# Kernel tuning notes

Measured on AMD Instinct MI355X. Metric: run time of the kernel, lower is better.

## Reference

```python
import jax, jax.numpy as jnp
import numpy as np

N_HEADS = 2

def setup_inputs() -> dict:
    key = jax.random.key(0)
    ks = jax.random.split(key, 10)
    d, bank, b, t = 192, 1000, 16, 4096
    s = 1.0 / np.sqrt(d)
    return {
        "z": jax.random.normal(ks[0], (b, d, t), jnp.float32),
        "memory_bank": jax.random.normal(ks[1], (d, bank), jnp.float32),
        "Wq": jax.random.normal(ks[2], (d, d), jnp.float32) * s,
        "bq": jax.random.normal(ks[3], (d,), jnp.float32) * 0.02,
        "Wk": jax.random.normal(ks[4], (d, d), jnp.float32) * s,
        "bk": jax.random.normal(ks[5], (d,), jnp.float32) * 0.02,
        "Wv": jax.random.normal(ks[6], (d, d), jnp.float32) * s,
        "bv": jax.random.normal(ks[7], (d,), jnp.float32) * 0.02,
        "Wo": jax.random.normal(ks[8], (d, d), jnp.float32) * s,
        "bo": jax.random.normal(ks[9], (d,), jnp.float32) * 0.02,
    }


def _split_heads(x):
    # x: [b, d, t] -> [b, h, t, dk]  (matches view(b, h, dk, t).transpose(2, 3))
    b, d, t = x.shape
    dk = d // N_HEADS
    return x.reshape(b, N_HEADS, dk, t).transpose(0, 1, 3, 2)


def reference(z, memory_bank, Wq, bq, Wk, bk, Wv, bv, Wo, bo):
    b, d, t = z.shape
    dk = d // N_HEADS
    # memory bank expanded over batch: [b, d, bank]
    c = jnp.broadcast_to(memory_bank[None], (b,) + memory_bank.shape)
    # 1x1 conv projections == per-channel linear
    q = jnp.einsum('oc,bct->bot', Wq, z) + bq[None, :, None]
    k = jnp.einsum('oc,bcs->bos', Wk, c) + bk[None, :, None]
    v = jnp.einsum('oc,bcs->bos', Wv, c) + bv[None, :, None]
    qh = _split_heads(q)  # [b, h, t, dk]
    kh = _split_heads(k)  # [b, h, bank, dk]
    vh = _split_heads(v)  # [b, h, bank, dk]
    scores = jnp.einsum('bhtd,bhsd->bhts', qh, kh) / jnp.sqrt(jnp.asarray(dk, z.dtype))
    p = jax.nn.softmax(scores, axis=-1)  # [b, h, t, bank]
    out = jnp.einsum('bhts,bhsd->bhtd', p, vh)  # [b, h, t, dk]
    out = out.transpose(0, 1, 3, 2).reshape(b, d, t)  # merge heads -> [b, d, t]
    return jnp.einsum('oc,bct->bot', Wo, out) + bo[None, :, None]
```

## Files before the change

### kernel.cpp

```cpp
#include <hip/hip_runtime.h>


typedef float  f32x4  __attribute__((ext_vector_type(4)));
typedef __bf16 bf16;
typedef __bf16 bf16x4 __attribute__((ext_vector_type(4)));
typedef __bf16 bf16x8 __attribute__((ext_vector_type(8)));

#define B_   16
#define D_   192
#define T_   4096
#define BANK 1000
#define SP   1024
#define DK   96
#define SCALE 0.10206207261596577f
#define LOG2E 1.4426950408889634f

__global__ __launch_bounds__(256) void pre_kernel(
    const float* __restrict__ z, bf16* __restrict__ zT,
    const float* __restrict__ mb,
    const float* __restrict__ Wk, const float* __restrict__ bk,
    const float* __restrict__ Wv, const float* __restrict__ bv,
    bf16* __restrict__ ktg, bf16* __restrict__ vtg) {
  __shared__ __align__(16) bf16 sT[64 * 200];
  const int tid = threadIdx.x;
  if (blockIdx.y < 16) {
    const int t0 = blockIdx.x * 64, b = blockIdx.y;
#pragma unroll
    for (int it = 0; it < 48; ++it) {
      int e = tid + 256 * it;
      int c = e >> 6, tl = e & 63;
      sT[tl * 200 + c] = (bf16)z[((size_t)b * D_ + c) * T_ + t0 + tl];
    }
    __syncthreads();
#pragma unroll
    for (int it = 0; it < 6; ++it) {
      int g = tid + 256 * it;
      int tl = g / 24, c8 = (g % 24) * 8;
      bf16x8 v = *(const bf16x8*)&sT[tl * 200 + c8];
      *(bf16x8*)&zT[((size_t)b * T_ + t0 + tl) * D_ + c8] = v;
    }
  } else {
    int idx = (blockIdx.y - 16) * 64 + blockIdx.x;
    int s = (idx & 3) * 256 + tid;
    int o = idx >> 2;
    int h = o / DK, i = o % DK;
    float ak = 0.f, av = 0.f;
    if (s < BANK) {
      ak = bk[o]; av = bv[o];
      for (int c = 0; c < D_; ++c) {
        float m = mb[c * BANK + s];
        ak += Wk[o * D_ + c] * m;
        av += Wv[o * D_ + c] * m;
      }
    }
    ktg[(size_t)(h * SP + s) * DK + i] = (bf16)ak;
    vtg[(size_t)(h * DK + i) * SP + s] = (bf16)av;
  }
}

template <typename OT>
__global__ __launch_bounds__(256) void proj_kernel(
    const bf16* __restrict__ XT, const float* __restrict__ W,
    const float* __restrict__ bias, OT* __restrict__ Y, float outscale) {
  __shared__ __align__(16) char smem[24576];
  bf16* sB = (bf16*)smem;
  float* sE = (float*)smem;

  const int tid = threadIdx.x;
  const int t0 = blockIdx.x * 256, o0 = blockIdx.y * 64, b = blockIdx.z;
  const int lane = tid & 63, wv = tid >> 6;
  const int quad = lane >> 4, l15 = lane & 15;

  const bf16* ap[4];
#pragma unroll
  for (int m = 0; m < 4; ++m)
    ap[m] = &XT[((size_t)b * T_ + t0 + (wv * 4 + m) * 16 + l15) * D_ + quad * 8];
  bf16x8 acur[4];
#pragma unroll
  for (int m = 0; m < 4; ++m) acur[m] = *(const bf16x8*)ap[m];

#pragma unroll
  for (int r = 0; r < 6; ++r) {
    int g = tid + 256 * r;
    int kb = g >> 8, nt = (g >> 6) & 3, qd = (g >> 4) & 3, l5 = g & 15;
    const float* wp = &W[(o0 + nt * 16 + l5) * D_ + kb * 32 + qd * 8];
    f32x4 wa = *(const f32x4*)wp, wb = *(const f32x4*)(wp + 4);
    bf16x8 pk;
#pragma unroll
    for (int u = 0; u < 4; ++u) { pk[u] = (bf16)wa[u]; pk[4 + u] = (bf16)wb[u]; }
    *(bf16x8*)&sB[(size_t)g * 8] = pk;
  }

  f32x4 acc[4][4];
#pragma unroll
  for (int m = 0; m < 4; ++m)
#pragma unroll
    for (int n = 0; n < 4; ++n) acc[m][n] = (f32x4){0.f, 0.f, 0.f, 0.f};

  __syncthreads();
  for (int kb = 0; kb < 6; ++kb) {
    bf16x8 anext[4];
    if (kb < 5) {
#pragma unroll
      for (int m = 0; m < 4; ++m)
        anext[m] = *(const bf16x8*)(ap[m] + (kb + 1) * 32);
    }
    bf16x8 bf[4];
#pragma unroll
    for (int n = 0; n < 4; ++n)
      bf[n] = *(const bf16x8*)&sB[(size_t)((kb * 4 + n) * 64 + lane) * 8];
#pragma unroll
    for (int m = 0; m < 4; ++m)
#pragma unroll
      for (int n = 0; n < 4; ++n)
        acc[m][n] = __builtin_amdgcn_mfma_f32_16x16x32_bf16(acur[m], bf[n], acc[m][n], 0, 0, 0);
    if (kb < 5) {
#pragma unroll
      for (int m = 0; m < 4; ++m) acur[m] = anext[m];
    }
  }
  __syncthreads();

  float bs[4];
#pragma unroll
  for (int n = 0; n < 4; ++n) bs[n] = bias[o0 + n * 16 + l15];
  float* se = sE + wv * 1088;
#pragma unroll
  for (int m = 0; m < 4; ++m) {
#pragma unroll
    for (int n = 0; n < 4; ++n)
#pragma unroll
      for (int r = 0; r < 4; ++r)
        se[(quad * 4 + r) * 68 + n * 16 + l15] = (acc[m][n][r] + bs[n]) * outscale;
#pragma unroll
    for (int oo = 0; oo < 16; ++oo) {
      int ol = oo * 4 + quad;
      Y[((size_t)b * D_ + o0 + ol) * T_ + t0 + wv * 64 + m * 16 + l15] =
          (OT)se[l15 * 68 + ol];
    }
  }
}

__global__ __launch_bounds__(512) void attn_kernel(
    const bf16* __restrict__ zT, const float* __restrict__ Wq,
    const float* __restrict__ bq, const bf16* __restrict__ ktg,
    const bf16* __restrict__ vtg, bf16* __restrict__ owsT) {
  __shared__ __align__(16) char smem[32768];
  bf16* kt = (bf16*)smem;
  bf16* vt = (bf16*)(smem + 12288);
  bf16* sP = (bf16*)(smem + 24576);
  bf16* qt = (bf16*)smem;

  const int tid = threadIdx.x;
  const int t0 = blockIdx.x * 128, h = blockIdx.y, b = blockIdx.z;
  const int lane = tid & 63, wv = tid >> 6;
  const int quad = lane >> 4, l15 = lane & 15;

  const bf16* kb_g = ktg + (size_t)h * SP * DK;
  const bf16* vb_g = vtg + (size_t)h * DK * SP;
  const bf16* sp_ptr[3];
  int sp_str[3];
#pragma unroll
  for (int r = 0; r < 3; ++r) {
    int g = tid + 512 * r;
    if (g < 768) {
      int kb = g >> 8, n = (g >> 6) & 3, qd = (g >> 4) & 3, l5 = g & 15;
      sp_ptr[r] = kb_g + (size_t)(n * 16 + l5) * DK + kb * 32 + qd * 8;
      sp_str[r] = 64 * DK;
    } else {
      int gv = g - 768, blk = gv >> 6;
      int kbv = blk / 6, n = blk % 6, qd = (gv >> 4) & 3, l5 = gv & 15;
      sp_ptr[r] = vb_g + (size_t)(n * 16 + l5) * SP + kbv * 32 + qd * 8;
      sp_str[r] = 64;
    }
  }
  bf16x8 kreg[3];
#pragma unroll
  for (int r = 0; r < 3; ++r) kreg[r] = *(const bf16x8*)sp_ptr[r];

  f32x4 qacc[6];
#pragma unroll
  for (int n = 0; n < 6; ++n) qacc[n] = (f32x4){0.f, 0.f, 0.f, 0.f};
  const bf16*  zrow = &zT[((size_t)b * T_ + t0 + wv * 16 + l15) * D_ + quad * 8];
  const float* wrow = &Wq[(size_t)(h * DK + l15) * D_ + quad * 8];
  for (int kb = 0; kb < 6; ++kb) {
    bf16x8 zf = *(const bf16x8*)(zrow + kb * 32);
#pragma unroll
    for (int n = 0; n < 6; ++n) {
      const float* wp = wrow + (size_t)n * 16 * D_ + kb * 32;
      f32x4 wa = *(const f32x4*)wp, wb = *(const f32x4*)(wp + 4);
      bf16x8 wf;
#pragma unroll
      for (int u = 0; u < 4; ++u) { wf[u] = (bf16)wa[u]; wf[4 + u] = (bf16)wb[u]; }
      qacc[n] = __builtin_amdgcn_mfma_f32_16x16x32_bf16(wf, zf, qacc[n], 0, 0, 0);
    }
  }
#pragma unroll
  for (int n = 0; n < 6; ++n) {
    f32x4 bq4 = *(const f32x4*)&bq[h * DK + n * 16 + quad * 4];
    int g = ((n & 1) * 2 + (quad >> 1)) * 16 + l15;
    int gs = g ^ ((g >> 3) & 7);
    bf16x4 pk;
#pragma unroll
    for (int r = 0; r < 4; ++r)
      pk[r] = (bf16)((qacc[n][r] + bq4[r]) * (SCALE * LOG2E));
    *(bf16x4*)&qt[(size_t)(((n >> 1) * 8 + wv) * 64 + gs) * 8 + (quad & 1) * 4] = pk;
  }
  bf16x8 qf[3];
#pragma unroll
  for (int kb = 0; kb < 3; ++kb)
    qf[kb] = *(const bf16x8*)&qt[(size_t)((kb * 8 + wv) * 64 + (lane ^ ((lane >> 3) & 7))) * 8];

  f32x4 oaccT[6];
#pragma unroll
  for (int n = 0; n < 6; ++n) oaccT[n] = (f32x4){0.f, 0.f, 0.f, 0.f};
  float m_run = -1e30f, l_run = 0.f;

  for (int ch = 0; ch < 16; ++ch) {
    __syncthreads();
#pragma unroll
    for (int r = 0; r < 3; ++r)
      *(bf16x8*)(smem + (size_t)(tid + 512 * r) * 16) = kreg[r];
    __syncthreads();
    if (ch < 15) {
#pragma unroll
      for (int r = 0; r < 3; ++r) {
        sp_ptr[r] += sp_str[r];
        kreg[r] = *(const bf16x8*)sp_ptr[r];
      }
    }

    f32x4 scT[4];
#pragma unroll
    for (int n = 0; n < 4; ++n) scT[n] = (f32x4){0.f, 0.f, 0.f, 0.f};
#pragma unroll
    for (int kb = 0; kb < 3; ++kb) {
#pragma unroll
      for (int n = 0; n < 4; ++n) {
        bf16x8 kf = *(const bf16x8*)&kt[(size_t)((kb * 4 + n) * 64 + lane) * 8];
        scT[n] = __builtin_amdgcn_mfma_f32_16x16x32_bf16(kf, qf[kb], scT[n], 0, 0, 0);
      }
    }
    if (ch == 15) {
#pragma unroll
      for (int r = 0; r < 4; ++r) {
        scT[3][r] = -1e30f;
        if (quad >= 2) scT[2][r] = -1e30f;
      }
    }

    float m0 = -1e30f;
#pragma unroll
    for (int n = 0; n < 4; ++n)
#pragma unroll
      for (int r = 0; r < 4; ++r) m0 = fmaxf(m0, scT[n][r]);
    m0 = fmaxf(m0, __shfl_xor(m0, 16, 64));
    m0 = fmaxf(m0, __shfl_xor(m0, 32, 64));
    if (!__all(m0 - m_run <= 8.f)) {
      float mn = fmaxf(m_run, m0);
      float al = exp2f(m_run - mn);
      m_run = mn;
      l_run *= al;
#pragma unroll
      for (int n = 0; n < 6; ++n)
#pragma unroll
        for (int r = 0; r < 4; ++r) oaccT[n][r] *= al;
    }
    float pr[4][4];
    float ls = 0.f;
#pragma unroll
    for (int n = 0; n < 4; ++n)
#pragma unroll
      for (int r = 0; r < 4; ++r) { pr[n][r] = exp2f(scT[n][r] - m_run); ls += pr[n][r]; }
    ls += __shfl_xor(ls, 16, 64);
    ls += __shfl_xor(ls, 32, 64);
    l_run += ls;

#pragma unroll
    for (int kb2 = 0; kb2 < 2; ++kb2) {
#pragma unroll
      for (int nh = 0; nh < 2; ++nh) {
        int n = kb2 * 2 + nh;
        int g = (nh * 2 + (quad >> 1)) * 16 + l15;
        int gs = g ^ ((g >> 3) & 7);
        bf16x4 pk = {(bf16)pr[n][0], (bf16)pr[n][1], (bf16)pr[n][2], (bf16)pr[n][3]};
        *(bf16x4*)&sP[(size_t)(wv * 64 + gs) * 8 + (quad & 1) * 4] = pk;
      }
      bf16x8 pa = *(const bf16x8*)&sP[(size_t)(wv * 64 + (lane ^ ((lane >> 3) & 7))) * 8];
#pragma unroll
      for (int n2 = 0; n2 < 6; ++n2) {
        bf16x8 vf = *(const bf16x8*)&vt[(size_t)((kb2 * 6 + n2) * 64 + lane) * 8];
        oaccT[n2] = __builtin_amdgcn_mfma_f32_16x16x32_bf16(vf, pa, oaccT[n2], 0, 0, 0);
      }
    }
  }

  float inv = 1.0f / l_run;
  bf16* orow = &owsT[((size_t)b * T_ + t0 + wv * 16 + l15) * D_ + h * DK + quad * 4];
#pragma unroll
  for (int n2 = 0; n2 < 6; ++n2) {
    bf16x4 pk = {(bf16)(oaccT[n2][0] * inv), (bf16)(oaccT[n2][1] * inv),
                 (bf16)(oaccT[n2][2] * inv), (bf16)(oaccT[n2][3] * inv)};
    *(bf16x4*)&orow[n2 * 16] = pk;
  }
}

extern "C" void kernel_launch(void* const* d_in, const int* in_sizes, int n_in,
                              void* d_out, int out_size, void* d_ws, size_t ws_size,
                              hipStream_t stream) {
  const float* z  = (const float*)d_in[0];
  const float* mb = (const float*)d_in[1];
  const float* Wq = (const float*)d_in[2];
  const float* bq = (const float*)d_in[3];
  const float* Wk = (const float*)d_in[4];
  const float* bk = (const float*)d_in[5];
  const float* Wv = (const float*)d_in[6];
  const float* bv = (const float*)d_in[7];
  const float* Wo = (const float*)d_in[8];
  const float* bo = (const float*)d_in[9];
  float* out = (float*)d_out;

  bf16* ktg  = (bf16*)d_ws;
  bf16* vtg  = ktg + 2 * SP * DK;
  bf16* zT   = vtg + 2 * DK * SP;
  bf16* owsT = zT + (size_t)B_ * T_ * D_;

  pre_kernel        <<<dim3(64, 28),          256, 0, stream>>>(z, zT, mb, Wk, bk, Wv, bv,
                                                                ktg, vtg);
  attn_kernel       <<<dim3(T_ / 128, 2, B_), 512, 0, stream>>>(zT, Wq, bq, ktg, vtg, owsT);
  proj_kernel<float><<<dim3(T_ / 256, 3, B_), 256, 0, stream>>>(owsT, Wo, bo, out, 1.0f);
}
```

Baseline: 268.6 us.

## Fuse z transpose into attention Q projection and vectorize output stores

The separate transpose-to-bf16 pass over z is removed; the attention kernel now reads fp32 z directly in column order and converts to bf16 while building MFMA fragments, so the zT workspace round-trip goes away. The K/V projection becomes its own small kernel. The output projection writes float4 vectors instead of scalar stores, and the softmax max and sum reductions become trees to shorten dependency chains. The strided per-element z loads in attention are coalesced across lanes, but each wave issues more load instructions and reads fp32 z twice (once per head).

```diff
diff --git a/kernel.cpp b/kernel.cpp
--- a/kernel.cpp
+++ b/kernel.cpp
@@ -15,53 +15,29 @@
 #define SCALE 0.10206207261596577f
 #define LOG2E 1.4426950408889634f
 
-__global__ __launch_bounds__(256) void pre_kernel(
-    const float* __restrict__ z, bf16* __restrict__ zT,
-    const float* __restrict__ mb,
-    const float* __restrict__ Wk, const float* __restrict__ bk,
+__global__ __launch_bounds__(256) void kv_kernel(
+    const float* __restrict__ mb, const float* __restrict__ Wk, const float* __restrict__ bk,
     const float* __restrict__ Wv, const float* __restrict__ bv,
     bf16* __restrict__ ktg, bf16* __restrict__ vtg) {
-  __shared__ __align__(16) bf16 sT[64 * 200];
-  const int tid = threadIdx.x;
-  if (blockIdx.y < 16) {
-    const int t0 = blockIdx.x * 64, b = blockIdx.y;
-#pragma unroll
-    for (int it = 0; it < 48; ++it) {
-      int e = tid + 256 * it;
-      int c = e >> 6, tl = e & 63;
-      sT[tl * 200 + c] = (bf16)z[((size_t)b * D_ + c) * T_ + t0 + tl];
-    }
-    __syncthreads();
-#pragma unroll
-    for (int it = 0; it < 6; ++it) {
-      int g = tid + 256 * it;
-      int tl = g / 24, c8 = (g % 24) * 8;
-      bf16x8 v = *(const bf16x8*)&sT[tl * 200 + c8];
-      *(bf16x8*)&zT[((size_t)b * T_ + t0 + tl) * D_ + c8] = v;
-    }
-  } else {
-    int idx = (blockIdx.y - 16) * 64 + blockIdx.x;
-    int s = (idx & 3) * 256 + tid;
-    int o = idx >> 2;
-    int h = o / DK, i = o % DK;
-    float ak = 0.f, av = 0.f;
-    if (s < BANK) {
-      ak = bk[o]; av = bv[o];
-      for (int c = 0; c < D_; ++c) {
-        float m = mb[c * BANK + s];
-        ak += Wk[o * D_ + c] * m;
-        av += Wv[o * D_ + c] * m;
-      }
-    }
-    ktg[(size_t)(h * SP + s) * DK + i] = (bf16)ak;
-    vtg[(size_t)(h * DK + i) * SP + s] = (bf16)av;
-  }
+  int s = blockIdx.x * 256 + threadIdx.x;
+  int o = blockIdx.y;
+  int h = o / DK, i = o % DK;
+  float ak = 0.f, av = 0.f;
+  if (s < BANK) {
+    ak = bk[o]; av = bv[o];
+    for (int c = 0; c < D_; ++c) {
+      float m = mb[c * BANK + s];
+      ak += Wk[o * D_ + c] * m;
+      av += Wv[o * D_ + c] * m;
+    }
+  }
+  ktg[(size_t)(h * SP + s) * DK + i] = (bf16)ak;
+  vtg[(size_t)(h * DK + i) * SP + s] = (bf16)av;
 }
 
-template <typename OT>
 __global__ __launch_bounds__(256) void proj_kernel(
     const bf16* __restrict__ XT, const float* __restrict__ W,
-    const float* __restrict__ bias, OT* __restrict__ Y, float outscale) {
+    const float* __restrict__ bias, float* __restrict__ Y) {
   __shared__ __align__(16) char smem[24576];
   bf16* sB = (bf16*)smem;
   float* sE = (float*)smem;
@@ -131,18 +107,20 @@
     for (int n = 0; n < 4; ++n)
 #pragma unroll
       for (int r = 0; r < 4; ++r)
-        se[(quad * 4 + r) * 68 + n * 16 + l15] = (acc[m][n][r] + bs[n]) * outscale;
-#pragma unroll
-    for (int oo = 0; oo < 16; ++oo) {
-      int ol = oo * 4 + quad;
-      Y[((size_t)b * D_ + o0 + ol) * T_ + t0 + wv * 64 + m * 16 + l15] =
-          (OT)se[l15 * 68 + ol];
+        se[(quad * 4 + r) * 68 + n * 16 + l15] = acc[m][n][r] + bs[n];
+#pragma unroll
+    for (int p = 0; p < 4; ++p) {
+      int o = p * 16 + (lane >> 2), tq = (lane & 3) * 4;
+      f32x4 vv;
+#pragma unroll
+      for (int u = 0; u < 4; ++u) vv[u] = se[(tq + u) * 68 + o];
+      *(f32x4*)&Y[((size_t)b * D_ + o0 + o) * T_ + t0 + wv * 64 + m * 16 + tq] = vv;
     }
   }
 }
 
 __global__ __launch_bounds__(512) void attn_kernel(
-    const bf16* __restrict__ zT, const float* __restrict__ Wq,
+    const float* __restrict__ z, const float* __restrict__ Wq,
     const float* __restrict__ bq, const bf16* __restrict__ ktg,
     const bf16* __restrict__ vtg, bf16* __restrict__ owsT) {
   __shared__ __align__(16) char smem[32768];
@@ -181,10 +159,13 @@
   f32x4 qacc[6];
 #pragma unroll
   for (int n = 0; n < 6; ++n) qacc[n] = (f32x4){0.f, 0.f, 0.f, 0.f};
-  const bf16*  zrow = &zT[((size_t)b * T_ + t0 + wv * 16 + l15) * D_ + quad * 8];
+  const float* zcol = &z[((size_t)b * D_ + quad * 8) * T_ + t0 + wv * 16 + l15];
   const float* wrow = &Wq[(size_t)(h * DK + l15) * D_ + quad * 8];
   for (int kb = 0; kb < 6; ++kb) {
-    bf16x8 zf = *(const bf16x8*)(zrow + kb * 32);
+    bf16x8 zf;
+#pragma unroll
+    for (int j = 0; j < 8; ++j)
+      zf[j] = (bf16)zcol[(size_t)(kb * 32 + j) * T_];
 #pragma unroll
     for (int n = 0; n < 6; ++n) {
       const float* wp = wrow + (size_t)n * 16 * D_ + kb * 32;
@@ -249,11 +230,13 @@
       }
     }
 
-    float m0 = -1e30f;
-#pragma unroll
-    for (int n = 0; n < 4; ++n)
-#pragma unroll
-      for (int r = 0; r < 4; ++r) m0 = fmaxf(m0, scT[n][r]);
+    float m8[8];
+#pragma unroll
+    for (int u = 0; u < 8; ++u)
+      m8[u] = fmaxf(scT[u >> 1][(u & 1) * 2], scT[u >> 1][(u & 1) * 2 + 1]);
+    float m4a = fmaxf(m8[0], m8[1]), m4b = fmaxf(m8[2], m8[3]);
+    float m4c = fmaxf(m8[4], m8[5]), m4d = fmaxf(m8[6], m8[7]);
+    float m0 = fmaxf(fmaxf(m4a, m4b), fmaxf(m4c, m4d));
     m0 = fmaxf(m0, __shfl_xor(m0, 16, 64));
     m0 = fmaxf(m0, __shfl_xor(m0, 32, 64));
     if (!__all(m0 - m_run <= 8.f)) {
@@ -267,11 +250,17 @@
         for (int r = 0; r < 4; ++r) oaccT[n][r] *= al;
     }
     float pr[4][4];
-    float ls = 0.f;
 #pragma unroll
     for (int n = 0; n < 4; ++n)
 #pragma unroll
-      for (int r = 0; r < 4; ++r) { pr[n][r] = exp2f(scT[n][r] - m_run); ls += pr[n][r]; }
+      for (int r = 0; r < 4; ++r) pr[n][r] = exp2f(scT[n][r] - m_run);
+    float s8[8];
+#pragma unroll
+    for (int u = 0; u < 8; ++u)
+      s8[u] = pr[u >> 1][(u & 1) * 2] + pr[u >> 1][(u & 1) * 2 + 1];
+    float s4a = s8[0] + s8[1], s4b = s8[2] + s8[3];
+    float s4c = s8[4] + s8[5], s4d = s8[6] + s8[7];
+    float ls = (s4a + s4b) + (s4c + s4d);
     ls += __shfl_xor(ls, 16, 64);
     ls += __shfl_xor(ls, 32, 64);
     l_run += ls;
@@ -322,11 +311,9 @@
 
   bf16* ktg  = (bf16*)d_ws;
   bf16* vtg  = ktg + 2 * SP * DK;
-  bf16* zT   = vtg + 2 * DK * SP;
-  bf16* owsT = zT + (size_t)B_ * T_ * D_;
-
-  pre_kernel        <<<dim3(64, 28),          256, 0, stream>>>(z, zT, mb, Wk, bk, Wv, bv,
-                                                                ktg, vtg);
-  attn_kernel       <<<dim3(T_ / 128, 2, B_), 512, 0, stream>>>(zT, Wq, bq, ktg, vtg, owsT);
-  proj_kernel<float><<<dim3(T_ / 256, 3, B_), 256, 0, stream>>>(owsT, Wo, bo, out, 1.0f);
+  bf16* owsT = vtg + 2 * DK * SP;
+
+  kv_kernel  <<<dim3(SP / 256, D_),    256, 0, stream>>>(mb, Wk, bk, Wv, bv, ktg, vtg);
+  attn_kernel<<<dim3(T_ / 128, 2, B_), 512, 0, stream>>>(z, Wq, bq, ktg, vtg, owsT);
+  proj_kernel<<<dim3(T_ / 256, 3, B_), 256, 0, stream>>>(owsT, Wo, bo, out);
 }
```

New measurement: 257.2 us. 1.04x faster.
